# Kernel optimization log

Measured on AMD Instinct MI355X. Metric: run time of the kernel, lower is better.

The kernel has to match this reference:

```python
import jax, jax.numpy as jnp
import numpy as np
import math

N_HEADS = 4


def setup_inputs() -> dict:
    key = jax.random.key(0)
    ks = jax.random.split(key, 5)
    Bs, M, T, C = 4, 190, 512, 64
    x = jax.random.normal(ks[0], (Bs, M, T, C), dtype=jnp.float32)
    s = 1.0 / math.sqrt(C)
    Wq = jax.random.normal(ks[1], (C, C), dtype=jnp.float32) * s
    Wk = jax.random.normal(ks[2], (C, C), dtype=jnp.float32) * s
    Wv = jax.random.normal(ks[3], (C, C), dtype=jnp.float32) * s
    Wp = jax.random.normal(ks[4], (C, C), dtype=jnp.float32) * s
    z = jnp.zeros((C,), dtype=jnp.float32)
    return {"x": x, "Wq": Wq, "bq": z, "Wk": Wk, "bk": z, "Wv": Wv, "bv": z, "Wp": Wp, "bp": z}


def reference(x, Wq, bq, Wk, bk, Wv, bv, Wp, bp):
    # AxialMultiAttention forward, tied=True, linear=False, dropout=0 (eval).
    Bs, M, T, C = x.shape
    N, D = N_HEADS, C // N_HEADS

    def heads(y):  # [Bs,M,T,C] -> [Bs,M,N,T,D]
        return y.reshape(Bs, M, T, N, D).transpose(0, 1, 3, 2, 4)

    q = heads(x @ Wq + bq)
    k = heads(x @ Wk + bk)
    v = heads(x @ Wv + bv)

    # tied: sum queries/keys over the axial (pair) dim M, keepdim -> size-1 axis
    q_t = q.sum(axis=1)  # [Bs,N,T,D]
    k_t = k.sum(axis=1)  # [Bs,N,T,D]
    scale = 1.0 / math.sqrt(D * M)
    weights = jax.nn.softmax(jnp.einsum('bnqd,bnkd->bnqk', q_t, k_t) * scale, axis=-1)  # [Bs,N,T,T]

    # broadcast tied weights across M when multiplying values
    att = jnp.einsum('bnqk,bmnkd->bmnqd', weights, v)  # [Bs,M,N,T,D]
    att = att.transpose(0, 1, 3, 2, 4).reshape(Bs, M, T, N * D)
    out = att @ Wp + bp  # [Bs,M,T,C]

    # a = weights.detach()[0].mean(0): weights has keepdim axis of size 1 in torch,
    # so [0] -> [1,N,T,T] and mean over dim 0 -> [N,T,T]
    a = jax.lax.stop_gradient(weights)[0]  # [N,T,T]
    return out, a
```

## Files before the change

### kernel.cpp

```cpp
#include <hip/hip_runtime.h>

typedef unsigned short ushort_t;
typedef __bf16 bf16x8 __attribute__((ext_vector_type(8)));
typedef float f32x4 __attribute__((ext_vector_type(4)));
typedef float f32x16 __attribute__((ext_vector_type(16)));

#define DEVI __device__ __forceinline__

constexpr int BSZ = 4;
constexpr int MDIM = 190;
constexpr int TDIM = 512;
constexpr int CDIM = 64;

DEVI ushort_t f2bf(float f) {
    union { float f; unsigned int u; } v; v.f = f;
    unsigned int u = v.u;
    u += 0x7FFFu + ((u >> 16) & 1u);
    return (ushort_t)(u >> 16);
}

__global__ __launch_bounds__(256, 4) void k_vproj(const float* __restrict__ x,
                                                  const float* __restrict__ Wv,
                                                  const float* __restrict__ bv,
                                                  ushort_t* __restrict__ vf,
                                                  float* __restrict__ xsp) {
    __shared__ __align__(16) ushort_t xbf[64 * 72];
    __shared__ __align__(16) ushort_t WvT[64 * 72];
    __shared__ __align__(16) ushort_t vst[64 * 72];

    int tid = threadIdx.x;
    int bid = blockIdx.x;
    int mg = bid & 15;
    int tt = (bid >> 4) & 7;
    int b = bid >> 7;
    int t0 = tt * 64;
    int mbase = mg * 12;
    int cnt = (mbase + 12 <= MDIM) ? 12 : (MDIM - mbase);

    int w = tid >> 6, lane = tid & 63;
    int la = lane & 15, lb = lane >> 4;
    int r = tid >> 2, seg = tid & 3;

    int chunk = tid >> 3, u = tid & 7;
    int ksr = chunk >> 3;
    int nn2 = (chunk >> 1) & 3;
    int lhi2 = chunk & 1;
    int d0 = u * 2;

#pragma unroll
    for (int rep = 0; rep < 16; ++rep) {
        int j = rep * 256 + tid;
        int ci = j >> 6, co = j & 63;
        WvT[co * 72 + ci] = f2bf(Wv[j]);
    }
    float bvv[4];
#pragma unroll
    for (int cf = 0; cf < 4; ++cf) bvv[cf] = bv[16 * cf + la];

    float xacc[16];
#pragma unroll
    for (int u2 = 0; u2 < 16; ++u2) xacc[u2] = 0.f;

    const size_t mstride = (size_t)TDIM * CDIM;
    size_t xaddr = ((size_t)(b * MDIM + mbase) * TDIM + t0 + r) * CDIM + seg * 16;

    float4 xv[4];
#pragma unroll
    for (int u2 = 0; u2 < 4; ++u2) xv[u2] = *(const float4*)(x + xaddr + u2 * 4);

    f32x4 zz = {0.f, 0.f, 0.f, 0.f};

    for (int i = 0; i < cnt; ++i) {
#pragma unroll
        for (int u2 = 0; u2 < 4; ++u2) {
            xacc[u2 * 4 + 0] += xv[u2].x;
            xacc[u2 * 4 + 1] += xv[u2].y;
            xacc[u2 * 4 + 2] += xv[u2].z;
            xacc[u2 * 4 + 3] += xv[u2].w;
            ushort4 h;
            h.x = f2bf(xv[u2].x); h.y = f2bf(xv[u2].y);
            h.z = f2bf(xv[u2].z); h.w = f2bf(xv[u2].w);
            *(ushort4*)&xbf[r * 72 + seg * 16 + u2 * 4] = h;
        }
        __syncthreads();

        int inext = (i + 1 < cnt) ? (i + 1) : i;
        size_t xaddr2 = xaddr + (size_t)(inext - i) * mstride;
        float4 xv2[4];
#pragma unroll
        for (int u2 = 0; u2 < 4; ++u2) xv2[u2] = *(const float4*)(x + xaddr2 + u2 * 4);

        f32x4 acc2[4];
#pragma unroll
        for (int cf = 0; cf < 4; ++cf) acc2[cf] = zz;
#pragma unroll
        for (int ks = 0; ks < 2; ++ks) {
            bf16x8 aa = *(const bf16x8*)&xbf[(w * 16 + la) * 72 + ks * 32 + lb * 8];
#pragma unroll
            for (int cf = 0; cf < 4; ++cf) {
                bf16x8 bb = *(const bf16x8*)&WvT[(16 * cf + la) * 72 + ks * 32 + lb * 8];
                acc2[cf] = __builtin_amdgcn_mfma_f32_16x16x32_bf16(aa, bb, acc2[cf], 0, 0, 0);
            }
        }
#pragma unroll
        for (int cf = 0; cf < 4; ++cf) {
            ushort4 h;
            h.x = f2bf(acc2[cf][0] + bvv[cf]);
            h.y = f2bf(acc2[cf][1] + bvv[cf]);
            h.z = f2bf(acc2[cf][2] + bvv[cf]);
            h.w = f2bf(acc2[cf][3] + bvv[cf]);
            *(ushort4*)&vst[(16 * cf + la) * 72 + w * 16 + lb * 4] = h;
        }
        __syncthreads();

        int m = mbase + i;
        int mblk = m >> 2, mrel = m & 3;
        int cg = mrel >> 1, half = mrel & 1;
        size_t vfbase = ((((size_t)(b * 48 + mblk) * 4 + nn2) * 32 + (tt * 4 + ksr)) * 2 + cg) * 512
                      + (size_t)(lhi2 * 32 + half * 16 + d0) * 8;
        uint4 v0 = *(const uint4*)&vst[(nn2 * 16 + d0) * 72 + ksr * 16 + lhi2 * 8];
        uint4 v1 = *(const uint4*)&vst[(nn2 * 16 + d0 + 1) * 72 + ksr * 16 + lhi2 * 8];
        *(uint4*)(vf + vfbase) = v0;
        *(uint4*)(vf + vfbase + 8) = v1;

#pragma unroll
        for (int u2 = 0; u2 < 4; ++u2) xv[u2] = xv2[u2];
        xaddr = xaddr2;
    }

    if (mg == 15) {
        uint4 z4 = {0u, 0u, 0u, 0u};
#pragma unroll
        for (int pm = 190; pm < 192; ++pm) {
            int mblk = pm >> 2, mrel = pm & 3;
            int cg = mrel >> 1, half = mrel & 1;
            size_t vfbase = ((((size_t)(b * 48 + mblk) * 4 + nn2) * 32 + (tt * 4 + ksr)) * 2 + cg) * 512
                          + (size_t)(lhi2 * 32 + half * 16 + d0) * 8;
            *(uint4*)(vf + vfbase) = z4;
            *(uint4*)(vf + vfbase + 8) = z4;
        }
    }

    size_t sbase = ((size_t)(mg * 4 + b) * TDIM + t0 + r) * CDIM + seg * 16;
#pragma unroll
    for (int u2 = 0; u2 < 4; ++u2) {
        float4 o;
        o.x = xacc[u2 * 4 + 0]; o.y = xacc[u2 * 4 + 1];
        o.z = xacc[u2 * 4 + 2]; o.w = xacc[u2 * 4 + 3];
        *(float4*)(xsp + sbase + u2 * 4) = o;
    }
}

__global__ __launch_bounds__(256) void k_xsum2(const float* __restrict__ xsp,
                                               const float* __restrict__ Wp,
                                               float* __restrict__ xsum,
                                               ushort_t* __restrict__ wpf) {
    int tid = threadIdx.x;
    int idx = blockIdx.x * 256 + tid;
    float s = 0.f;
#pragma unroll
    for (int p = 0; p < 16; ++p) s += xsp[(size_t)p * 131072 + idx];
    xsum[idx] = s;

    if (blockIdx.x == 0) {
#pragma unroll
        for (int rp = 0; rp < 16; ++rp) {
            int u = rp * 256 + tid;
            int cf = u >> 11, kk = (u >> 9) & 3, lf = (u >> 3) & 63, j = u & 7;
            wpf[u] = f2bf(Wp[(kk * 16 + (lf >> 5) * 8 + j) * 64 + cf * 32 + (lf & 31)]);
        }
    }
}

__global__ __launch_bounds__(256) void k_weights(const float* __restrict__ xsum,
                                                 const float* __restrict__ Wq,
                                                 const float* __restrict__ bq,
                                                 const float* __restrict__ Wk,
                                                 const float* __restrict__ bk,
                                                 ushort_t* __restrict__ wf,
                                                 float* __restrict__ a_out) {
    __shared__ __align__(16) float kt[512][20];
    __shared__ __align__(16) float qt[32][20];
    __shared__ __align__(16) float xs[64][68];
    __shared__ __align__(16) float wcol[64][16];
    __shared__ float kbias[16], qbias[16];
    __shared__ __align__(16) ushort_t rowbuf[32][520];

    int tid = threadIdx.x;
    int bid = blockIdx.x;
    int tcn = bid & 15;
    int n = (bid >> 4) & 3;
    int b = bid >> 6;
    int t0 = tcn * 32;

    for (int j = tid; j < 1024; j += 256) {
        int c = j >> 4, d = j & 15;
        wcol[c][d] = Wk[c * 64 + n * 16 + d];
    }
    if (tid < 16) kbias[tid] = 190.0f * bk[n * 16 + tid];
    if (tid >= 16 && tid < 32) qbias[tid - 16] = 190.0f * bq[n * 16 + tid - 16];
    __syncthreads();

    for (int ch = 0; ch < 8; ++ch) {
        for (int j = tid; j < 4096; j += 256) {
            int t = j >> 6, c = j & 63;
            xs[t][c] = xsum[((size_t)(b * 512) + (ch * 64 + t)) * 64 + c];
        }
        __syncthreads();
#pragma unroll
        for (int o = 0; o < 4; ++o) {
            int oi = o * 256 + tid;
            int t = oi >> 4, d = oi & 15;
            float s = 0.f;
#pragma unroll
            for (int c = 0; c < 64; ++c) s += xs[t][c] * wcol[c][d];
            kt[ch * 64 + t][d] = s + kbias[d];
        }
        __syncthreads();
    }

    for (int j = tid; j < 1024; j += 256) {
        int c = j >> 4, d = j & 15;
        wcol[c][d] = Wq[c * 64 + n * 16 + d];
    }
    for (int j = tid; j < 2048; j += 256) {
        int t = j >> 6, c = j & 63;
        xs[t][c] = xsum[((size_t)(b * 512) + (t0 + t)) * 64 + c];
    }
    __syncthreads();
#pragma unroll
    for (int o = 0; o < 2; ++o) {
        int oi = o * 256 + tid;
        int t = oi >> 4, d = oi & 15;
        float s = 0.f;
#pragma unroll
        for (int c = 0; c < 64; ++c) s += xs[t][c] * wcol[c][d];
        qt[t][d] = s + qbias[d];
    }
    __syncthreads();

    const float scale = 0.01813692f;
    int w = tid >> 6, lane = tid & 63;
    for (int rr = 0; rr < 8; ++rr) {
        int r = w * 8 + rr;
        float qreg[16];
#pragma unroll
        for (int d = 0; d < 16; ++d) qreg[d] = qt[r][d];
        float lv[8];
#pragma unroll
        for (int i = 0; i < 8; ++i) {
            int k = lane + 64 * i;
            const float* kr = &kt[k][0];
            float s = 0.f;
#pragma unroll
            for (int d = 0; d < 16; ++d) s += qreg[d] * kr[d];
            lv[i] = s * scale;
        }
        float mx = lv[0];
#pragma unroll
        for (int i = 1; i < 8; ++i) mx = fmaxf(mx, lv[i]);
#pragma unroll
        for (int off = 32; off >= 1; off >>= 1) mx = fmaxf(mx, __shfl_xor(mx, off));
        float se = 0.f;
#pragma unroll
        for (int i = 0; i < 8; ++i) { lv[i] = __expf(lv[i] - mx); se += lv[i]; }
#pragma unroll
        for (int off = 32; off >= 1; off >>= 1) se += __shfl_xor(se, off);
        float inv = 1.0f / se;

        size_t abase = ((size_t)(n * 512 + (t0 + r))) * 512;
#pragma unroll
        for (int i = 0; i < 8; ++i) {
            float wv = lv[i] * inv;
            rowbuf[r][lane + 64 * i] = f2bf(wv);
            if (b == 0) a_out[abase + lane + 64 * i] = wv;
        }
    }
    __syncthreads();

    size_t wfbase = ((size_t)((b * 4 + n) * 16 + tcn)) * 32 * 512;
#pragma unroll
    for (int p = 0; p < 8; ++p) {
        int id = p * 256 + tid;
        int ks = id >> 6;
        int lf = id & 63;
        int l31 = lf & 31, lhi = lf >> 5;
        uint4 v = *(const uint4*)&rowbuf[l31][ks * 16 + lhi * 8];
        *(uint4*)(wf + wfbase + (size_t)ks * 512 + lf * 8) = v;
    }
}

__global__ __launch_bounds__(512, 2) void k_att(const ushort_t* __restrict__ wf,
                                                const ushort_t* __restrict__ vf,
                                                const ushort_t* __restrict__ wpf,
                                                const float* __restrict__ bp,
                                                float* __restrict__ out) {
    __shared__ __align__(16) ushort_t attS[32768];

    int tid = threadIdx.x;
    int bid0 = blockIdx.x;
    int bid = (bid0 & 7) * 48 + (bid0 >> 3);
    int mq = bid % 24;
    int panel = bid / 24;
    int tt = panel & 3;
    int b = panel >> 2;

    int wid = tid >> 6, lane = tid & 63;
    int l31 = lane & 31, lhi = lane >> 5;
    int n = wid >> 1;
    int mh = wid & 1;
    int mblk = mq * 2 + mh;

    unsigned abase[4];
#pragma unroll
    for (int q = 0; q < 4; ++q)
        abase[q] = (unsigned)((((b * 4 + n) * 16 + tt * 4 + q) * 32) * 512 + lane * 8);
    unsigned bbase[2];
#pragma unroll
    for (int j = 0; j < 2; ++j)
        bbase[j] = (unsigned)(((((b * 48 + mblk) * 4 + n) * 32) * 2 + j) * 512 + lane * 8);

    f32x16 acc[4][2];
#pragma unroll
    for (int q = 0; q < 4; ++q)
#pragma unroll
        for (int j = 0; j < 2; ++j) acc[q][j] = (f32x16)(0.f);

    bf16x8 Ae[4], Be[2], Ao[4], Bo[2];

#define LOADC(A_, B_, KS) do {                                                    \
    _Pragma("unroll")                                                             \
    for (int q = 0; q < 4; ++q)                                                   \
        A_[q] = *(const bf16x8*)(wf + abase[q] + (KS) * 512);                     \
    _Pragma("unroll")                                                             \
    for (int j = 0; j < 2; ++j)                                                   \
        B_[j] = *(const bf16x8*)(vf + bbase[j] + (KS) * 1024);                    \
} while (0)

#define COMPC(A_, B_) do {                                                        \
    _Pragma("unroll")                                                             \
    for (int j = 0; j < 2; ++j)                                                   \
        _Pragma("unroll")                                                         \
        for (int q = 0; q < 4; ++q)                                               \
            acc[q][j] = __builtin_amdgcn_mfma_f32_32x32x16_bf16(A_[q], B_[j], acc[q][j], 0, 0, 0); \
} while (0)

#define VMW(N) do { asm volatile("s_waitcnt vmcnt(" #N ")" ::: "memory"); __builtin_amdgcn_sched_barrier(0); } while (0)

    LOADC(Ae, Be, 0);
    LOADC(Ao, Bo, 1);
#pragma unroll
    for (int kc = 0; kc < 30; kc += 2) {
        VMW(6);  COMPC(Ae, Be);  LOADC(Ae, Be, kc + 2);
        VMW(6);  COMPC(Ao, Bo);  LOADC(Ao, Bo, kc + 3);
    }
    VMW(6);  COMPC(Ae, Be);
    VMW(0);  COMPC(Ao, Bo);
#undef LOADC
#undef COMPC
#undef VMW

    float bpv[2];
#pragma unroll
    for (int cf = 0; cf < 2; ++cf) bpv[cf] = bp[cf * 32 + l31];

    int mloc2 = wid >> 1;
    int th2 = wid & 1;

#pragma unroll
    for (int h = 0; h < 2; ++h) {
        __syncthreads();
        if (mh == h) {
            int mloc = ((l31 >> 4));
            int d = l31 & 15;
#pragma unroll
            for (int cg = 0; cg < 2; ++cg)
#pragma unroll
                for (int q = 0; q < 4; ++q) {
                    f32x16 a = acc[q][cg];
                    int ml = cg * 2 + mloc;
#pragma unroll
                    for (int r = 0; r < 16; ++r) {
                        int tl = q * 32 + (r & 3) + 8 * (r >> 2) + 4 * lhi;
                        int idx = (((ml * 128 + tl) * 64) + n * 16 + d) ^ ((tl & 7) << 3);
                        attS[idx] = f2bf(a[r]);
                    }
                }
        }
        __syncthreads();

        f32x16 acc2[2][2];
#pragma unroll
        for (int q2 = 0; q2 < 2; ++q2)
#pragma unroll
            for (int cf = 0; cf < 2; ++cf) acc2[q2][cf] = (f32x16)(0.f);
#pragma unroll
        for (int kk = 0; kk < 4; ++kk) {
            bf16x8 bbf[2];
#pragma unroll
            for (int cf = 0; cf < 2; ++cf)
                bbf[cf] = *(const bf16x8*)(wpf + (cf * 4 + kk) * 512 + lane * 8);
#pragma unroll
            for (int q2 = 0; q2 < 2; ++q2) {
                int tl = th2 * 64 + q2 * 32 + l31;
                int aidx = (((mloc2 * 128 + tl) * 64) + kk * 16 + lhi * 8) ^ ((tl & 7) << 3);
                bf16x8 aa = *(const bf16x8*)(attS + aidx);
#pragma unroll
                for (int cf = 0; cf < 2; ++cf)
                    acc2[q2][cf] = __builtin_amdgcn_mfma_f32_32x32x16_bf16(aa, bbf[cf], acc2[q2][cf], 0, 0, 0);
            }
        }
        int m = mq * 8 + h * 4 + mloc2;
        if (m < 190) {
            size_t obase = ((size_t)(b * 190 + m) * 512 + tt * 128 + th2 * 64) * 64;
#pragma unroll
            for (int q2 = 0; q2 < 2; ++q2)
#pragma unroll
                for (int cf = 0; cf < 2; ++cf)
#pragma unroll
                    for (int r = 0; r < 16; ++r) {
                        int ts = q2 * 32 + (r & 3) + 8 * (r >> 2) + 4 * lhi;
                        out[obase + (size_t)ts * 64 + cf * 32 + l31] = acc2[q2][cf][r] + bpv[cf];
                    }
        }
    }
}

extern "C" void kernel_launch(void* const* d_in, const int* in_sizes, int n_in,
                              void* d_out, int out_size, void* d_ws, size_t ws_size,
                              hipStream_t stream) {
    const float* x  = (const float*)d_in[0];
    const float* Wq = (const float*)d_in[1];
    const float* bq = (const float*)d_in[2];
    const float* Wk = (const float*)d_in[3];
    const float* bk = (const float*)d_in[4];
    const float* Wv = (const float*)d_in[5];
    const float* bv = (const float*)d_in[6];
    const float* Wp = (const float*)d_in[7];
    const float* bp = (const float*)d_in[8];

    float* out = (float*)d_out;
    float* a_out = out + (size_t)BSZ * MDIM * TDIM * CDIM;

    float* xsp = out;

    float* xsum = (float*)d_ws;
    ushort_t* wf = (ushort_t*)((char*)d_ws + 524288);
    ushort_t* vf = (ushort_t*)((char*)d_ws + 524288 + 8388608);
    ushort_t* wpf = (ushort_t*)((char*)d_ws + 524288 + 8388608 + 50331648);

    k_vproj<<<512, 256, 0, stream>>>(x, Wv, bv, vf, xsp);
    k_xsum2<<<512, 256, 0, stream>>>(xsp, Wp, xsum, wpf);
    k_weights<<<256, 256, 0, stream>>>(xsum, Wq, bq, Wk, bk, wf, a_out);
    k_att<<<384, 512, 0, stream>>>(wf, vf, wpf, bp, out);
}
```

Before: 140.6 us.

## Restructure attention kernel into smaller blocks with LDS-staged V pipeline

```diff
diff --git a/kernel.cpp b/kernel.cpp
--- a/kernel.cpp
+++ b/kernel.cpp
@@ -17,6 +17,12 @@
     unsigned int u = v.u;
     u += 0x7FFFu + ((u >> 16) & 1u);
     return (ushort_t)(u >> 16);
+}
+
+DEVI void gload16(ushort_t* ldsBase, const ushort_t* g) {
+    __builtin_amdgcn_global_load_lds(
+        (const __attribute__((address_space(1))) unsigned int*)g,
+        (__attribute__((address_space(3))) unsigned int*)ldsBase, 16, 0, 0);
 }
 
 __global__ __launch_bounds__(256, 4) void k_vproj(const float* __restrict__ x,
@@ -290,139 +296,166 @@
     }
 }
 
-__global__ __launch_bounds__(512, 2) void k_att(const ushort_t* __restrict__ wf,
+__global__ __launch_bounds__(256, 3) void k_att(const ushort_t* __restrict__ wf,
                                                 const ushort_t* __restrict__ vf,
                                                 const ushort_t* __restrict__ wpf,
                                                 const float* __restrict__ bp,
                                                 float* __restrict__ out) {
-    __shared__ __align__(16) ushort_t attS[32768];
+    __shared__ __align__(16) ushort_t lds[24576];
 
     int tid = threadIdx.x;
     int bid0 = blockIdx.x;
-    int bid = (bid0 & 7) * 48 + (bid0 >> 3);
-    int mq = bid % 24;
-    int panel = bid / 24;
-    int tt = panel & 3;
-    int b = panel >> 2;
-
-    int wid = tid >> 6, lane = tid & 63;
+    int bid = (bid0 & 7) * 192 + (bid0 >> 3);
+    int tt = bid & 7;
+    int mq = (bid >> 3) % 48;
+    int b = bid / 384;
+
+    int w = tid >> 6, lane = tid & 63;
     int l31 = lane & 31, lhi = lane >> 5;
-    int n = wid >> 1;
-    int mh = wid & 1;
-    int mblk = mq * 2 + mh;
-
-    unsigned abase[4];
-#pragma unroll
-    for (int q = 0; q < 4; ++q)
-        abase[q] = (unsigned)((((b * 4 + n) * 16 + tt * 4 + q) * 32) * 512 + lane * 8);
-    unsigned bbase[2];
-#pragma unroll
-    for (int j = 0; j < 2; ++j)
-        bbase[j] = (unsigned)(((((b * 48 + mblk) * 4 + n) * 32) * 2 + j) * 512 + lane * 8);
-
-    f32x16 acc[4][2];
-#pragma unroll
-    for (int q = 0; q < 4; ++q)
+    int n = w;
+
+    unsigned abase[2];
+#pragma unroll
+    for (int q = 0; q < 2; ++q)
+        abase[q] = (unsigned)((((b * 4 + n) * 16 + tt * 2 + q) * 32) * 512 + lane * 8);
+    unsigned vbase = (unsigned)(((b * 48 + mq) * 4 + n) * 32768 + lane * 8);
+    int nbase = n * 6144;
+    ushort_t* vwave = lds + nbase;
+
+    f32x16 acc[2][2];
+#pragma unroll
+    for (int q = 0; q < 2; ++q)
 #pragma unroll
         for (int j = 0; j < 2; ++j) acc[q][j] = (f32x16)(0.f);
 
-    bf16x8 Ae[4], Be[2], Ao[4], Bo[2];
-
-#define LOADC(A_, B_, KS) do {                                                    \
+    bf16x8 We[2][2], Wo[2][2];
+
+#define WLOAD(W_, P) do {                                                         \
     _Pragma("unroll")                                                             \
-    for (int q = 0; q < 4; ++q)                                                   \
-        A_[q] = *(const bf16x8*)(wf + abase[q] + (KS) * 512);                     \
+    for (int kk = 0; kk < 2; ++kk)                                                \
+        _Pragma("unroll")                                                         \
+        for (int q = 0; q < 2; ++q)                                               \
+            W_[kk][q] = *(const bf16x8*)(wf + abase[q] + ((P) * 2 + kk) * 512);   \
+} while (0)
+
+#define VLOAD(P) do {                                                             \
     _Pragma("unroll")                                                             \
-    for (int j = 0; j < 2; ++j)                                                   \
-        B_[j] = *(const bf16x8*)(vf + bbase[j] + (KS) * 1024);                    \
+    for (int kk = 0; kk < 2; ++kk)                                                \
+        _Pragma("unroll")                                                         \
+        for (int cg = 0; cg < 2; ++cg)                                            \
+            gload16(vwave + ((P) % 3) * 2048 + kk * 1024 + cg * 512,              \
+                    vf + vbase + ((P) * 2 + kk) * 1024 + cg * 512);               \
 } while (0)
 
-#define COMPC(A_, B_) do {                                                        \
+#define SB __builtin_amdgcn_sched_barrier(0)
+#define VMW4 do { asm volatile("s_waitcnt vmcnt(4)" ::: "memory"); SB; } while (0)
+#define VMW0 do { asm volatile("s_waitcnt vmcnt(0)" ::: "memory"); SB; } while (0)
+
+#define MM(W_, P) do {                                                            \
+    bf16x8 Bv[2][2];                                                              \
     _Pragma("unroll")                                                             \
-    for (int j = 0; j < 2; ++j)                                                   \
+    for (int kk = 0; kk < 2; ++kk)                                                \
         _Pragma("unroll")                                                         \
-        for (int q = 0; q < 4; ++q)                                               \
-            acc[q][j] = __builtin_amdgcn_mfma_f32_32x32x16_bf16(A_[q], B_[j], acc[q][j], 0, 0, 0); \
+        for (int cg = 0; cg < 2; ++cg)                                            \
+            Bv[kk][cg] = *(const bf16x8*)(vwave + ((P) % 3) * 2048 + kk * 1024 + cg * 512 + lane * 8); \
+    SB;                                                                           \
+    if ((P) < 15) { if ((P) & 1) WLOAD(We, (P) + 1); else WLOAD(Wo, (P) + 1); }   \
+    SB;                                                                           \
+    if ((P) < 14) VLOAD((P) + 2);                                                 \
+    SB;                                                                           \
+    _Pragma("unroll")                                                             \
+    for (int kk = 0; kk < 2; ++kk)                                                \
+        _Pragma("unroll")                                                         \
+        for (int q = 0; q < 2; ++q)                                               \
+            _Pragma("unroll")                                                     \
+            for (int cg = 0; cg < 2; ++cg)                                        \
+                acc[q][cg] = __builtin_amdgcn_mfma_f32_32x32x16_bf16(W_[kk][q], Bv[kk][cg], acc[q][cg], 0, 0, 0); \
 } while (0)
 
-#define VMW(N) do { asm volatile("s_waitcnt vmcnt(" #N ")" ::: "memory"); __builtin_amdgcn_sched_barrier(0); } while (0)
-
-    LOADC(Ae, Be, 0);
-    LOADC(Ao, Bo, 1);
-#pragma unroll
-    for (int kc = 0; kc < 30; kc += 2) {
-        VMW(6);  COMPC(Ae, Be);  LOADC(Ae, Be, kc + 2);
-        VMW(6);  COMPC(Ao, Bo);  LOADC(Ao, Bo, kc + 3);
-    }
-    VMW(6);  COMPC(Ae, Be);
-    VMW(0);  COMPC(Ao, Bo);
-#undef LOADC
-#undef COMPC
-#undef VMW
+    WLOAD(We, 0); SB;
+    VLOAD(0); SB;
+    VLOAD(1); SB;
+
+    VMW4; MM(We, 0);
+    VMW4; MM(Wo, 1);
+    VMW4; MM(We, 2);
+    VMW4; MM(Wo, 3);
+    VMW4; MM(We, 4);
+    VMW4; MM(Wo, 5);
+    VMW4; MM(We, 6);
+    VMW4; MM(Wo, 7);
+    VMW4; MM(We, 8);
+    VMW4; MM(Wo, 9);
+    VMW4; MM(We, 10);
+    VMW4; MM(Wo, 11);
+    VMW4; MM(We, 12);
+    VMW4; MM(Wo, 13);
+    VMW4; MM(We, 14);
+    VMW0; MM(Wo, 15);
+
+#undef WLOAD
+#undef VLOAD
+#undef VMW4
+#undef VMW0
+#undef MM
+#undef SB
 
     float bpv[2];
 #pragma unroll
     for (int cf = 0; cf < 2; ++cf) bpv[cf] = bp[cf * 32 + l31];
 
-    int mloc2 = wid >> 1;
-    int th2 = wid & 1;
-
-#pragma unroll
-    for (int h = 0; h < 2; ++h) {
-        __syncthreads();
-        if (mh == h) {
-            int mloc = ((l31 >> 4));
-            int d = l31 & 15;
-#pragma unroll
-            for (int cg = 0; cg < 2; ++cg)
-#pragma unroll
-                for (int q = 0; q < 4; ++q) {
-                    f32x16 a = acc[q][cg];
-                    int ml = cg * 2 + mloc;
-#pragma unroll
-                    for (int r = 0; r < 16; ++r) {
-                        int tl = q * 32 + (r & 3) + 8 * (r >> 2) + 4 * lhi;
-                        int idx = (((ml * 128 + tl) * 64) + n * 16 + d) ^ ((tl & 7) << 3);
-                        attS[idx] = f2bf(a[r]);
-                    }
+    __syncthreads();
+    {
+        int d = l31 & 15;
+        int mlh = l31 >> 4;
+#pragma unroll
+        for (int cg = 0; cg < 2; ++cg)
+#pragma unroll
+            for (int q = 0; q < 2; ++q) {
+                f32x16 a = acc[q][cg];
+                int ml = cg * 2 + mlh;
+#pragma unroll
+                for (int r = 0; r < 16; ++r) {
+                    int tl = q * 32 + (r & 3) + 8 * (r >> 2) + 4 * lhi;
+                    lds[(((ml * 64 + tl) * 64) + n * 16 + d) ^ ((tl & 7) << 3)] = f2bf(a[r]);
                 }
-        }
-        __syncthreads();
-
-        f32x16 acc2[2][2];
+            }
+    }
+    __syncthreads();
+
+    f32x16 acc2[2][2];
+#pragma unroll
+    for (int q2 = 0; q2 < 2; ++q2)
+#pragma unroll
+        for (int cf = 0; cf < 2; ++cf) acc2[q2][cf] = (f32x16)(0.f);
+#pragma unroll
+    for (int kk = 0; kk < 4; ++kk) {
+        bf16x8 bbf[2];
+#pragma unroll
+        for (int cf = 0; cf < 2; ++cf)
+            bbf[cf] = *(const bf16x8*)(wpf + (cf * 4 + kk) * 512 + lane * 8);
+#pragma unroll
+        for (int q2 = 0; q2 < 2; ++q2) {
+            int tl = q2 * 32 + l31;
+            int aoff = (((w * 64 + tl) * 64) + kk * 16 + lhi * 8) ^ ((tl & 7) << 3);
+            bf16x8 aa = *(const bf16x8*)(lds + aoff);
+#pragma unroll
+            for (int cf = 0; cf < 2; ++cf)
+                acc2[q2][cf] = __builtin_amdgcn_mfma_f32_32x32x16_bf16(aa, bbf[cf], acc2[q2][cf], 0, 0, 0);
+        }
+    }
+    int m = mq * 4 + w;
+    if (m < 190) {
+        size_t obase = ((size_t)(b * 190 + m) * 512 + tt * 64) * 64;
 #pragma unroll
         for (int q2 = 0; q2 < 2; ++q2)
 #pragma unroll
-            for (int cf = 0; cf < 2; ++cf) acc2[q2][cf] = (f32x16)(0.f);
-#pragma unroll
-        for (int kk = 0; kk < 4; ++kk) {
-            bf16x8 bbf[2];
-#pragma unroll
             for (int cf = 0; cf < 2; ++cf)
-                bbf[cf] = *(const bf16x8*)(wpf + (cf * 4 + kk) * 512 + lane * 8);
-#pragma unroll
-            for (int q2 = 0; q2 < 2; ++q2) {
-                int tl = th2 * 64 + q2 * 32 + l31;
-                int aidx = (((mloc2 * 128 + tl) * 64) + kk * 16 + lhi * 8) ^ ((tl & 7) << 3);
-                bf16x8 aa = *(const bf16x8*)(attS + aidx);
-#pragma unroll
-                for (int cf = 0; cf < 2; ++cf)
-                    acc2[q2][cf] = __builtin_amdgcn_mfma_f32_32x32x16_bf16(aa, bbf[cf], acc2[q2][cf], 0, 0, 0);
-            }
-        }
-        int m = mq * 8 + h * 4 + mloc2;
-        if (m < 190) {
-            size_t obase = ((size_t)(b * 190 + m) * 512 + tt * 128 + th2 * 64) * 64;
-#pragma unroll
-            for (int q2 = 0; q2 < 2; ++q2)
-#pragma unroll
-                for (int cf = 0; cf < 2; ++cf)
-#pragma unroll
-                    for (int r = 0; r < 16; ++r) {
-                        int ts = q2 * 32 + (r & 3) + 8 * (r >> 2) + 4 * lhi;
-                        out[obase + (size_t)ts * 64 + cf * 32 + l31] = acc2[q2][cf][r] + bpv[cf];
-                    }
-        }
+#pragma unroll
+                for (int r = 0; r < 16; ++r) {
+                    int ts = q2 * 32 + (r & 3) + 8 * (r >> 2) + 4 * lhi;
+                    out[obase + (size_t)ts * 64 + cf * 32 + l31] = acc2[q2][cf][r] + bpv[cf];
+                }
     }
 }
 
@@ -452,5 +485,5 @@
     k_vproj<<<512, 256, 0, stream>>>(x, Wv, bv, vf, xsp);
     k_xsum2<<<512, 256, 0, stream>>>(xsp, Wp, xsum, wpf);
     k_weights<<<256, 256, 0, stream>>>(xsum, Wq, bq, Wk, bk, wf, a_out);
-    k_att<<<384, 512, 0, stream>>>(wf, vf, wpf, bp, out);
-}
+    k_att<<<1536, 256, 0, stream>>>(wf, vf, wpf, bp, out);
+}
```

Result: faster. 120.7 us (-14.1%).
